# Performance work log

Hardware: AMD Instinct MI355X
Metric: run time of the kernel (lower is better)

Reference implementation:

```python
import jax, jax.numpy as jnp
import numpy as np

Q = 8
T, N, M = 16, 128, 128
K = 5
C_IN = 2 + T            # x, y, and T solution timesteps stacked as channels
C_HID = 2 * (4 + Q)     # 24
C_OUT = 4 + Q           # kappa, v1, v2, f, q RK-stage fields
DT = 1.0


def _conv(h, W, b):
    # h: (C, N, M), W: (O, C, K, K) -> (O, N, M), SAME padding (padding = K//2)
    o = jax.lax.conv_general_dilated(h[None], W, (1, 1), 'SAME',
                                     dimension_numbers=('NCHW', 'OIHW', 'NCHW'))[0]
    return o + b[:, None, None]


def setup_inputs() -> dict:
    key = jax.random.key(0)
    ks = jax.random.split(key, 12)
    def w(k, o, c):
        return jax.random.normal(k, (o, c, K, K), jnp.float32) * (1.0 / np.sqrt(c * K * K))
    return {
        'x': jax.random.normal(ks[0], (N, M), jnp.float32),
        'y': jax.random.normal(ks[1], (N, M), jnp.float32),
        'u': jax.random.normal(ks[2], (T, N, M), jnp.float32),
        'W1': w(ks[3], C_HID, C_IN), 'b1': jnp.zeros((C_HID,), jnp.float32),
        'W2': w(ks[4], C_HID, C_HID), 'b2': jnp.zeros((C_HID,), jnp.float32),
        'W3': w(ks[5], C_HID, C_HID), 'b3': jnp.zeros((C_HID,), jnp.float32),
        'W4': w(ks[6], C_HID, C_HID), 'b4': jnp.zeros((C_HID,), jnp.float32),
        'W5': w(ks[7], C_OUT, C_HID), 'b5': jnp.zeros((C_OUT,), jnp.float32),
        'rk_A': jax.random.normal(ks[8], (Q, Q), jnp.float32) * 0.05,
        'rk_b': jax.random.normal(ks[9], (Q,), jnp.float32) * 0.05,
    }


def reference(x, y, u, W1, b1, W2, b2, W3, b3, W4, b4, W5, b5, rk_A, rk_b):
    def net(xx, yy):
        h = jnp.concatenate([xx[None], yy[None], u], axis=0)  # (2+T, N, M)
        h = jax.nn.relu(_conv(h, W1, b1))
        h = jax.nn.relu(_conv(h, W2, b2))
        h = jax.nn.relu(_conv(h, W3, b3))
        h = jax.nn.relu(_conv(h, W4, b4))
        return _conv(h, W5, b5)  # (C_OUT, N, M)

    outs, vjp = jax.vjp(net, x, y)
    kappa, v1, v2, f = outs[0], outs[1], outs[2], outs[3]
    u_rk = outs[4:]  # (Q, N, M)

    # one-hot channel cotangents for kappa, v1, v2 and the Q RK-stage fields
    idx = jnp.array([0, 1, 2] + list(range(4, 4 + Q)))
    n_cot = idx.shape[0]
    cots = jnp.zeros((n_cot, C_OUT, N, M), outs.dtype).at[jnp.arange(n_cot), idx].set(1.0)

    # batched first-order VJPs (replaces the torch autograd.grad loop)
    gx, gy = jax.vmap(vjp)(cots)
    kappa_x, v1_x, v2_x = gx[0], gx[1], gx[2]
    kappa_y, v1_y, v2_y = gy[0], gy[1], gy[2]
    u_rk_x, u_rk_y = gx[3:], gy[3:]  # (Q, N, M)

    ones = jnp.ones((N, M), outs.dtype)
    cot_u = cots[3:]

    def du_x(xx, c):
        return jax.vjp(lambda a: net(a, y), xx)[1](c)[0]

    def du_y(yy, c):
        return jax.vjp(lambda a: net(x, a), yy)[1](c)[0]

    # second derivatives: VJP of the first-derivative map, batched over RK stages
    u_rk_xx = jax.vmap(lambda c: jax.vjp(lambda a: du_x(a, c), x)[1](ones)[0])(cot_u)
    u_rk_yy = jax.vmap(lambda c: jax.vjp(lambda a: du_y(a, c), y)[1](ones)[0])(cot_u)

    pde = (kappa[None] * (u_rk_xx + u_rk_yy)
           + kappa_x[None] * u_rk_x + kappa_y[None] * u_rk_y
           + v1[None] * u_rk_x + v2[None] * u_rk_y
           + f[None])

    uhat_i = u_rk + DT * jnp.einsum('ij,jkl->ikl', rk_A, pde)
    uhat_f = u_rk + DT * jnp.einsum('ij,jkl->ikl', rk_A - rk_b[None, :], pde)

    # all outputs of the torch forward, stacked along channel dim: (2Q+10, N, M)
    return jnp.concatenate([
        uhat_i, uhat_f,
        kappa[None], kappa_x[None], kappa_y[None],
        v1[None], v1_x[None], v1_y[None],
        v2[None], v2_x[None], v2_y[None],
        f[None]], axis=0)
```

## Files before the change

kernel.cpp:

```cpp
#include <hip/hip_runtime.h>

static constexpr int P = 16384;

static constexpr int OFF_H1   = 0;
static constexpr int OFF_H2   = 24 * P;
static constexpr int OFF_H3   = 48 * P;
static constexpr int OFF_H4   = 72 * P;
static constexpr int OFF_OUT5 = 96 * P;
static constexpr int OFF_GA   = 108 * P;
static constexpr int OFF_GB   = 372 * P;
static constexpr int OFF_DXY  = 636 * P;
static constexpr int OFF_W    = 658 * P;

static constexpr int PW1 = 0;
static constexpr int PW2 = 10800;
static constexpr int PW3 = 25200;
static constexpr int PW4 = 39600;
static constexpr int PW5 = 54000;
static constexpr int PB4 = 61200;
static constexpr int PB3 = 75600;
static constexpr int PB2 = 90000;
static constexpr int PB1 = 104400;

__global__ void pack_weights(const float* __restrict__ W1, const float* __restrict__ W2,
                             const float* __restrict__ W3, const float* __restrict__ W4,
                             const float* __restrict__ W5, float* __restrict__ wp,
                             float* __restrict__ tbl) {
    int i = blockIdx.x * 256 + threadIdx.x;
    if (i < 10800) {
        int co = i % 24, ci = (i / 24) % 18, t = i / 432;
        wp[PW1 + i] = W1[(co * 18 + ci) * 25 + t];
    }
    if (i < 14400) {
        int co = i % 24, ci = (i / 24) % 24, t = i / 576;
        wp[PW2 + i] = W2[(co * 24 + ci) * 25 + t];
        wp[PW3 + i] = W3[(co * 24 + ci) * 25 + t];
        wp[PW4 + i] = W4[(co * 24 + ci) * 25 + t];
        int cin = i % 24, cout = (i / 24) % 24, tb = i / 576;
        wp[PB4 + i] = W4[(cout * 24 + cin) * 25 + (24 - tb)];
        wp[PB3 + i] = W3[(cout * 24 + cin) * 25 + (24 - tb)];
        wp[PB2 + i] = W2[(cout * 24 + cin) * 25 + (24 - tb)];
    }
    if (i < 7200) {
        int co = i % 12, ci = (i / 12) % 24, t = i / 288;
        wp[PW5 + i] = W5[(co * 24 + ci) * 25 + t];
    }
    if (i < 1200) {
        int ci = i % 2, co = (i / 2) % 24, t = i / 48;
        wp[PB1 + i] = W1[(co * 18 + ci) * 25 + (24 - t)];
    }
    if (i < 6600) {
        int cx = i % 5, cy = (i / 5) % 5, ci = (i / 25) % 24, cot = i / 600;
        int oc = (cot < 3) ? cot : cot + 1;
        int a0 = (cy <= 2) ? 0 : cy - 2, a1 = (cy >= 2) ? 4 : cy + 2;
        int b0 = (cx <= 2) ? 0 : cx - 2, b1 = (cx >= 2) ? 4 : cx + 2;
        const float* __restrict__ w = W5 + (oc * 24 + ci) * 25;
        float s = 0.f;
        for (int a = a0; a <= a1; ++a)
            for (int b = b0; b <= b1; ++b) s += w[a * 5 + b];
        tbl[i] = s;
    }
}

__global__ void stage_input(const float* __restrict__ x, const float* __restrict__ y,
                            const float* __restrict__ u, float* __restrict__ in18) {
    int i = blockIdx.x * 256 + threadIdx.x;
    int pl = i / P, p = i - pl * P;
    float v = (pl == 0) ? x[p] : (pl == 1) ? y[p] : u[(pl - 2) * P + p];
    in18[i] = v;
}

template <int NTY, int TW, int SW, int CIN, int CHUNK, int COUT_TOT, int COB,
          bool RELU, bool MASK, bool BATCH, bool TBL>
__global__ __launch_bounds__(NTY * TW, 7) void conv5x5(
    const float* __restrict__ inbase, const float* __restrict__ wp,
    const float* __restrict__ bias, const float* __restrict__ maskbase,
    const float* __restrict__ tbl, float* __restrict__ outbase) {
    constexpr int NSPL = COUT_TOT / COB;
    constexpr int TR = NTY;
    constexpr int HR = TR + 4;
    constexpr int HC = TW + 4;
    constexpr int NT = NTY * TW;
    constexpr int HTOT = HR * HC;
    constexpr int NSLOT = (HTOT + NT - 1) / NT;
    const int z = blockIdx.z;
    const int half = z % NSPL;
    const int cot = z / NSPL;
    const float* in = inbase + ((BATCH && !TBL) ? cot * CIN * P : 0);
    float* out = outbase + (BATCH ? cot * COUT_TOT * P : 0);
    const int cobase = half * COB;

    __shared__ float smem[CHUNK][HR][SW];
    const int tid = threadIdx.x;
    const int bx = blockIdx.x, by = blockIdx.y;
    const int ty = tid / TW, tx = tid % TW;

    bool s_store[NSLOT];
    bool s_valid[NSLOT];
    int  s_goff[NSLOT];
    int  s_lds[NSLOT];
    int  s_tcls[NSLOT];
#pragma unroll
    for (int s = 0; s < NSLOT; ++s) {
        int i = tid + s * NT;
        int r = i / HC, c = i % HC;
        int gy = by * TR + r - 2, gx = bx * TW + c - 2;
        s_store[s] = (i < HTOT);
        s_valid[s] = (i < HTOT) && ((unsigned)gy < 128u) && ((unsigned)gx < 128u);
        s_goff[s]  = gy * 128 + gx;
        s_lds[s]   = r * SW + c;
        if (TBL) {
            int cy = (gy < 2) ? gy : (gy > 125) ? gy - 123 : 2;
            int cx = (gx < 2) ? gx : (gx > 125) ? gx - 123 : 2;
            s_tcls[s] = cy * 5 + cx;
        }
    }

    float acc[COB];
#pragma unroll
    for (int co = 0; co < COB; ++co) acc[co] = bias ? bias[cobase + co] : 0.f;

    for (int c0 = 0; c0 < CIN; c0 += CHUNK) {
        if (c0) __syncthreads();
#pragma unroll
        for (int s = 0; s < NSLOT; ++s) {
            if (s_store[s]) {
                float* lbase = &smem[0][0][0] + s_lds[s];
                const float* gbase = in + c0 * P + s_goff[s];
#pragma unroll
                for (int ci = 0; ci < CHUNK; ++ci) {
                    float v = 0.f;
                    if (s_valid[s]) {
                        if (TBL) {
                            float m = gbase[ci * P];
                            if (m > 0.f)
                                v = tbl[(cot * CIN + c0 + ci) * 25 + s_tcls[s]];
                        } else {
                            v = gbase[ci * P];
                        }
                    }
                    lbase[ci * HR * SW] = v;
                }
            }
        }
        __syncthreads();

        for (int a = 0; a < 5; ++a) {
            for (int b = 0; b < 5; ++b) {
                const float* __restrict__ wrow =
                    wp + ((a * 5 + b) * CIN + c0) * COUT_TOT + cobase;
                for (int ci = 0; ci < CHUNK; ++ci) {
                    float v = smem[ci][ty + a][tx + b];
#pragma unroll
                    for (int co = 0; co < COB; ++co)
                        acc[co] = fmaf(v, wrow[ci * COUT_TOT + co], acc[co]);
                }
            }
        }
    }

    const int gy = by * TR + ty, gx = bx * TW + tx, gp = gy * 128 + gx;
#pragma unroll
    for (int co = 0; co < COB; ++co) {
        float v = acc[co];
        if (RELU) v = v > 0.f ? v : 0.f;
        if (MASK) v = (maskbase[(cobase + co) * P + gp] > 0.f) ? v : 0.f;
        out[(cobase + co) * P + gp] = v;
    }
}

__global__ __launch_bounds__(256) void finalize(const float* __restrict__ ws,
                                                const float* __restrict__ rkA,
                                                const float* __restrict__ rkb,
                                                float* __restrict__ outp) {
    const int p = blockIdx.x * 256 + threadIdx.x;
    const float* o5 = ws + OFF_OUT5;
    const float* dxy = ws + OFF_DXY;

    const float kap = o5[0 * P + p], v1 = o5[1 * P + p];
    const float v2  = o5[2 * P + p], f  = o5[3 * P + p];
    const float kx  = dxy[0 * P + p], ky  = dxy[1 * P + p];
    const float v1x = dxy[2 * P + p], v1y = dxy[3 * P + p];
    const float v2x = dxy[4 * P + p], v2y = dxy[5 * P + p];
    const float cx = kx + v1, cy = ky + v2;

    float pde[8], urk[8];
#pragma unroll
    for (int q = 0; q < 8; ++q) {
        urk[q] = o5[(4 + q) * P + p];
        float ux = dxy[(6 + 2 * q) * P + p];
        float uy = dxy[(7 + 2 * q) * P + p];
        pde[q] = fmaf(cx, ux, fmaf(cy, uy, f));
    }
#pragma unroll
    for (int r = 0; r < 8; ++r) {
        float si = 0.f, sf = 0.f;
#pragma unroll
        for (int j = 0; j < 8; ++j) {
            float a = rkA[r * 8 + j];
            si = fmaf(a, pde[j], si);
            sf = fmaf(a - rkb[j], pde[j], sf);
        }
        outp[r * P + p] = urk[r] + si;
        outp[(8 + r) * P + p] = urk[r] + sf;
    }
    outp[16 * P + p] = kap;
    outp[17 * P + p] = kx;
    outp[18 * P + p] = ky;
    outp[19 * P + p] = v1;
    outp[20 * P + p] = v1x;
    outp[21 * P + p] = v1y;
    outp[22 * P + p] = v2;
    outp[23 * P + p] = v2x;
    outp[24 * P + p] = v2y;
    outp[25 * P + p] = f;
}

extern "C" void kernel_launch(void* const* d_in, const int* in_sizes, int n_in,
                              void* d_out, int out_size, void* d_ws, size_t ws_size,
                              hipStream_t stream) {
    const float* x   = (const float*)d_in[0];
    const float* y   = (const float*)d_in[1];
    const float* u   = (const float*)d_in[2];
    const float* W1  = (const float*)d_in[3];
    const float* b1  = (const float*)d_in[4];
    const float* W2  = (const float*)d_in[5];
    const float* b2  = (const float*)d_in[6];
    const float* W3  = (const float*)d_in[7];
    const float* b3  = (const float*)d_in[8];
    const float* W4  = (const float*)d_in[9];
    const float* b4  = (const float*)d_in[10];
    const float* W5  = (const float*)d_in[11];
    const float* b5  = (const float*)d_in[12];
    const float* rkA = (const float*)d_in[13];
    const float* rkb = (const float*)d_in[14];

    float* ws   = (float*)d_ws;
    float* outp = (float*)d_out;
    float* wp   = ws + OFF_W;
    float* tbl  = ws + OFF_GA;

    pack_weights<<<dim3(57), dim3(256), 0, stream>>>(W1, W2, W3, W4, W5, wp, tbl);
    stage_input<<<dim3(18 * 64), dim3(256), 0, stream>>>(x, y, u, ws + OFF_GB);

    dim3 blk256(256);
    conv5x5<16, 16, 24, 18, 9, 24, 4, true, false, false, false>
        <<<dim3(8, 8, 6), blk256, 0, stream>>>(
        ws + OFF_GB, wp + PW1, b1, nullptr, nullptr, ws + OFF_H1);
    conv5x5<16, 16, 24, 24, 12, 24, 4, true, false, false, false>
        <<<dim3(8, 8, 6), blk256, 0, stream>>>(
        ws + OFF_H1, wp + PW2, b2, nullptr, nullptr, ws + OFF_H2);
    conv5x5<16, 16, 24, 24, 12, 24, 4, true, false, false, false>
        <<<dim3(8, 8, 6), blk256, 0, stream>>>(
        ws + OFF_H2, wp + PW3, b3, nullptr, nullptr, ws + OFF_H3);
    conv5x5<16, 16, 24, 24, 12, 24, 4, true, false, false, false>
        <<<dim3(8, 8, 6), blk256, 0, stream>>>(
        ws + OFF_H3, wp + PW4, b4, nullptr, nullptr, ws + OFF_H4);
    conv5x5<16, 16, 24, 24, 12, 12, 4, false, false, false, false>
        <<<dim3(8, 8, 3), blk256, 0, stream>>>(
        ws + OFF_H4, wp + PW5, b5, nullptr, nullptr, ws + OFF_OUT5);

    conv5x5<16, 16, 24, 24, 12, 24, 12, false, true, true, true>
        <<<dim3(8, 8, 22), blk256, 0, stream>>>(
        ws + OFF_H4, wp + PB4, nullptr, ws + OFF_H3, tbl, ws + OFF_GB);
    conv5x5<16, 16, 24, 24, 12, 24, 12, false, true, true, false>
        <<<dim3(8, 8, 22), blk256, 0, stream>>>(
        ws + OFF_GB, wp + PB3, nullptr, ws + OFF_H2, nullptr, ws + OFF_GA);
    conv5x5<16, 16, 24, 24, 12, 24, 12, false, true, true, false>
        <<<dim3(8, 8, 22), blk256, 0, stream>>>(
        ws + OFF_GA, wp + PB2, nullptr, ws + OFF_H1, nullptr, ws + OFF_GB);
    conv5x5<16, 16, 24, 24, 12, 2, 2, false, false, true, false>
        <<<dim3(8, 8, 11), blk256, 0, stream>>>(
        ws + OFF_GB, wp + PB1, nullptr, nullptr, nullptr, ws + OFF_DXY);

    finalize<<<dim3(64), blk256, 0, stream>>>(ws, rkA, rkb, outp);
}
```

Before: 564.9 us.

## Prefetch next input chunk into registers during conv compute

```diff
diff --git a/kernel.cpp b/kernel.cpp
--- a/kernel.cpp
+++ b/kernel.cpp
@@ -72,7 +72,7 @@
 
 template <int NTY, int TW, int SW, int CIN, int CHUNK, int COUT_TOT, int COB,
           bool RELU, bool MASK, bool BATCH, bool TBL>
-__global__ __launch_bounds__(NTY * TW, 7) void conv5x5(
+__global__ __launch_bounds__(NTY * TW, 6) void conv5x5(
     const float* __restrict__ inbase, const float* __restrict__ wp,
     const float* __restrict__ bias, const float* __restrict__ maskbase,
     const float* __restrict__ tbl, float* __restrict__ outbase) {
@@ -83,6 +83,8 @@
     constexpr int NT = NTY * TW;
     constexpr int HTOT = HR * HC;
     constexpr int NSLOT = (HTOT + NT - 1) / NT;
+    constexpr int NCHUNK = CIN / CHUNK;
+    static_assert(CIN % CHUNK == 0, "CHUNK must divide CIN");
     const int z = blockIdx.z;
     const int half = z % NSPL;
     const int cot = z / NSPL;
@@ -107,7 +109,7 @@
         int gy = by * TR + r - 2, gx = bx * TW + c - 2;
         s_store[s] = (i < HTOT);
         s_valid[s] = (i < HTOT) && ((unsigned)gy < 128u) && ((unsigned)gx < 128u);
-        s_goff[s]  = gy * 128 + gx;
+        s_goff[s]  = s_valid[s] ? (gy * 128 + gx) : 0;
         s_lds[s]   = r * SW + c;
         if (TBL) {
             int cy = (gy < 2) ? gy : (gy > 125) ? gy - 123 : 2;
@@ -116,34 +118,50 @@
         }
     }
 
-    float acc[COB];
-#pragma unroll
-    for (int co = 0; co < COB; ++co) acc[co] = bias ? bias[cobase + co] : 0.f;
-
-    for (int c0 = 0; c0 < CIN; c0 += CHUNK) {
-        if (c0) __syncthreads();
+    float rv[NSLOT][CHUNK];
+
+    auto load_chunk = [&](int c0) {
+#pragma unroll
+        for (int s = 0; s < NSLOT; ++s) {
+            const float* gb = in + c0 * P + s_goff[s];
+#pragma unroll
+            for (int ci = 0; ci < CHUNK; ++ci) rv[s][ci] = gb[ci * P];
+        }
+    };
+    auto write_chunk = [&](int c0) {
 #pragma unroll
         for (int s = 0; s < NSLOT; ++s) {
             if (s_store[s]) {
-                float* lbase = &smem[0][0][0] + s_lds[s];
-                const float* gbase = in + c0 * P + s_goff[s];
+                float* lb = &smem[0][0][0] + s_lds[s];
 #pragma unroll
                 for (int ci = 0; ci < CHUNK; ++ci) {
                     float v = 0.f;
                     if (s_valid[s]) {
                         if (TBL) {
-                            float m = gbase[ci * P];
-                            if (m > 0.f)
+                            if (rv[s][ci] > 0.f)
                                 v = tbl[(cot * CIN + c0 + ci) * 25 + s_tcls[s]];
                         } else {
-                            v = gbase[ci * P];
+                            v = rv[s][ci];
                         }
                     }
-                    lbase[ci * HR * SW] = v;
+                    lb[ci * HR * SW] = v;
                 }
             }
         }
-        __syncthreads();
+    };
+
+    float acc[COB];
+#pragma unroll
+    for (int co = 0; co < COB; ++co) acc[co] = bias ? bias[cobase + co] : 0.f;
+
+    load_chunk(0);
+    write_chunk(0);
+    __syncthreads();
+
+#pragma unroll
+    for (int k = 0; k < NCHUNK; ++k) {
+        const int c0 = k * CHUNK;
+        if (k + 1 < NCHUNK) load_chunk(c0 + CHUNK);
 
         for (int a = 0; a < 5; ++a) {
             for (int b = 0; b < 5; ++b) {
@@ -156,6 +174,12 @@
                         acc[co] = fmaf(v, wrow[ci * COUT_TOT + co], acc[co]);
                 }
             }
+        }
+
+        if (k + 1 < NCHUNK) {
+            __syncthreads();
+            write_chunk(c0 + CHUNK);
+            __syncthreads();
         }
     }
 
```

Measured after the change: 912.2 us. +61.5%, slower.
